# Optimization experiments

Measured on AMD Instinct MI355X. Metric: run time of the kernel, lower is better.

## Reference

```python
import jax, jax.numpy as jnp
import numpy as np

MEX_C = 2.0 / (np.sqrt(3.0) * np.pi ** 0.25)

def mexican_hat(z):
    return MEX_C * (z * z - 1.0) * jnp.exp(-0.5 * z * z)

def setup_inputs() -> dict:
    key = jax.random.key(0)
    ks = jax.random.split(key, 5)
    B, T, D, O = 4, 2048, 128, 128
    x = jax.random.normal(ks[0], (B, T, D), dtype=jnp.float32)
    # init like torch: scale ~ U(0.5,1.5), translation ~ U(-0.5,0.5), kaiming-ish weights
    scale = jax.random.uniform(ks[1], (O, D), dtype=jnp.float32, minval=0.5, maxval=1.5)
    translation = jax.random.uniform(ks[2], (O, D), dtype=jnp.float32, minval=-0.5, maxval=0.5)
    bound = 1.0 / np.sqrt(D)
    wavelet_weights = jax.random.uniform(ks[3], (O, D), dtype=jnp.float32, minval=-bound, maxval=bound)
    base_w = jax.random.uniform(ks[4], (O, D), dtype=jnp.float32, minval=-bound, maxval=bound)
    ln_gamma = jnp.ones((D,), dtype=jnp.float32)
    ln_beta = jnp.zeros((D,), dtype=jnp.float32)
    return {"x": x, "scale": scale, "translation": translation,
            "wavelet_weights": wavelet_weights, "base_w": base_w,
            "ln_gamma": ln_gamma, "ln_beta": ln_beta}

def reference(x, scale, translation, wavelet_weights, base_w, ln_gamma, ln_beta):
    B, T, D = x.shape
    O = wavelet_weights.shape[0]
    # LayerNorm over last dim (eps = 1e-5, torch default)
    mu = jnp.mean(x, axis=-1, keepdims=True)
    var = jnp.mean((x - mu) ** 2, axis=-1, keepdims=True)
    x_norm = (x - mu) / jnp.sqrt(var + 1e-5) * ln_gamma + ln_beta
    x_flat = x_norm.reshape(B * T, D)                      # (N, D)
    s = jax.nn.softplus(scale) + 0.1                       # (O, D)
    # broadcast intermediate (N, O, D) — the memory-bound path
    z = (x_flat[:, None, :] - translation[None]) / s[None]
    w = jnp.clip(mexican_hat(z), -10.0, 10.0)              # (N, O, D)
    wavelet_out = jnp.einsum('nod,od->no', w, wavelet_weights)
    base_out = x.reshape(B * T, D) @ base_w.T              # base uses raw x
    out = wavelet_out + jax.nn.silu(base_out)
    return out.reshape(B, T, O)
```

## Files before the change

### kernel.cpp

```cpp
#include <hip/hip_runtime.h>


#define D_DIM 128
#define O_DIM 128
#define ROWS  16
#define BLOCK 1024

#define C1     0.72134752f
#define SQRT_C 0.84932180f
#define WWK    1.2023651f
#define LOG2E  1.44269504f

__global__ __launch_bounds__(256) void wavekan_prep(
    const float* __restrict__ scale,
    const float* __restrict__ trans,
    const float* __restrict__ ww,
    const float* __restrict__ bw,
    float4* __restrict__ wsW)
{
    int idx = blockIdx.x * blockDim.x + threadIdx.x;
    if (idx >= O_DIM * D_DIM) return;
    int o = idx >> 7;
    int d = idx & (D_DIM - 1);
    float sc = scale[idx];
    float sp = fmaxf(sc, 0.0f) + log1pf(__expf(-fabsf(sc)));
    float is2 = SQRT_C / (sp + 0.1f);
    float4 w;
    w.x = trans[idx] * is2;
    w.y = is2;
    w.z = ww[idx] * WWK;
    w.w = bw[idx];
    wsW[d * O_DIM + o] = w;
}

template<bool USE_WS>
__global__ __launch_bounds__(BLOCK, 8) void wavekan_main(
    const float* __restrict__ x,
    const float* __restrict__ scale,
    const float* __restrict__ trans,
    const float* __restrict__ ww,
    const float* __restrict__ bw,
    const float* __restrict__ gamma,
    const float* __restrict__ beta,
    const float4* __restrict__ wsW,
    float* __restrict__ out,
    int N)
{
    __shared__ float2 s_lr[ROWS * D_DIM];

    const int tid  = threadIdx.x;
    const int row0 = blockIdx.x * ROWS;

    {
        const int r  = tid >> 6;
        const int j  = tid & 63;
        const int d0 = j * 2;
        const int grow = row0 + r;

        float2 v2 = make_float2(0.f, 0.f);
        if (grow < N)
            v2 = *reinterpret_cast<const float2*>(x + (size_t)grow * D_DIM + d0);

        float sum = v2.x + v2.y;
        float ssq = v2.x * v2.x + v2.y * v2.y;
        #pragma unroll
        for (int m = 1; m < 64; m <<= 1) {
            sum += __shfl_xor(sum, m, 64);
            ssq += __shfl_xor(ssq, m, 64);
        }
        const float mean = sum * (1.0f / D_DIM);
        const float var  = ssq * (1.0f / D_DIM) - mean * mean;
        const float rstd = rsqrtf(var + 1e-5f);

        float2 g2 = *reinterpret_cast<const float2*>(gamma + d0);
        float2 b2 = *reinterpret_cast<const float2*>(beta + d0);

        s_lr[r * D_DIM + d0]     = make_float2((v2.x - mean) * rstd * g2.x + b2.x, v2.x);
        s_lr[r * D_DIM + d0 + 1] = make_float2((v2.y - mean) * rstd * g2.y + b2.y, v2.y);
    }
    __syncthreads();

    const int o = tid & (O_DIM - 1);
    const int g = tid >> 7;
    const float2* __restrict__ lr = s_lr + g * 2 * D_DIM;

    float accw0 = 0.f, accw1 = 0.f, accb0 = 0.f, accb1 = 0.f;

    if (USE_WS) {
        float4 w = wsW[o];
        #pragma unroll 4
        for (int d = 0; d < D_DIM; ++d) {
            float4 wn = wsW[(((d + 1) & (D_DIM - 1)) << 7) + o];
            float2 v0 = lr[d];
            float2 v1 = lr[D_DIM + d];

            float u0 = fmaf(v0.x, w.y, -w.x);
            float u1 = fmaf(v1.x, w.y, -w.x);
            float q0 = u0 * u0;
            float q1 = u1 * u1;
            float e0 = __builtin_amdgcn_exp2f(-q0);
            float e1 = __builtin_amdgcn_exp2f(-q1);
            accw0 = fmaf((q0 - C1) * e0, w.z, accw0);
            accw1 = fmaf((q1 - C1) * e1, w.z, accw1);
            accb0 = fmaf(v0.y, w.w, accb0);
            accb1 = fmaf(v1.y, w.w, accb1);
            w = wn;
        }
    } else {
        for (int d = 0; d < D_DIM; ++d) {
            int idx = o * D_DIM + d;
            float sc = scale[idx];
            float sp = fmaxf(sc, 0.0f) + log1pf(__expf(-fabsf(sc)));
            float is  = SQRT_C / (sp + 0.1f);
            float tws = trans[idx] * is;
            float wwk = ww[idx] * WWK;
            float bwv = bw[idx];
            float2 v0 = lr[d];
            float2 v1 = lr[D_DIM + d];
            float u0 = fmaf(v0.x, is, -tws);
            float u1 = fmaf(v1.x, is, -tws);
            float q0 = u0 * u0;
            float q1 = u1 * u1;
            accw0 = fmaf((q0 - C1) * __builtin_amdgcn_exp2f(-q0), wwk, accw0);
            accw1 = fmaf((q1 - C1) * __builtin_amdgcn_exp2f(-q1), wwk, accw1);
            accb0 = fmaf(v0.y, bwv, accb0);
            accb1 = fmaf(v1.y, bwv, accb1);
        }
    }

    {
        const int rr0 = row0 + g * 2;
        if (rr0 < N) {
            float sig0 = 1.0f / (1.0f + __builtin_amdgcn_exp2f(-LOG2E * accb0));
            out[(size_t)rr0 * O_DIM + o] = accw0 + accb0 * sig0;
        }
        if (rr0 + 1 < N) {
            float sig1 = 1.0f / (1.0f + __builtin_amdgcn_exp2f(-LOG2E * accb1));
            out[(size_t)(rr0 + 1) * O_DIM + o] = accw1 + accb1 * sig1;
        }
    }
}

extern "C" void kernel_launch(void* const* d_in, const int* in_sizes, int n_in,
                              void* d_out, int out_size, void* d_ws, size_t ws_size,
                              hipStream_t stream) {
    const float* x     = (const float*)d_in[0];
    const float* scale = (const float*)d_in[1];
    const float* trans = (const float*)d_in[2];
    const float* ww    = (const float*)d_in[3];
    const float* bw    = (const float*)d_in[4];
    const float* gamma = (const float*)d_in[5];
    const float* beta  = (const float*)d_in[6];
    float* out = (float*)d_out;

    const int N = in_sizes[0] / D_DIM;
    const int grid = (N + ROWS - 1) / ROWS;

    const size_t ws_needed = (size_t)O_DIM * D_DIM * sizeof(float4);
    if (ws_size >= ws_needed) {
        wavekan_prep<<<(O_DIM * D_DIM + 255) / 256, 256, 0, stream>>>(
            scale, trans, ww, bw, (float4*)d_ws);
        wavekan_main<true><<<grid, BLOCK, 0, stream>>>(
            x, scale, trans, ww, bw, gamma, beta, (const float4*)d_ws, out, N);
    } else {
        wavekan_main<false><<<grid, BLOCK, 0, stream>>>(
            x, scale, trans, ww, bw, gamma, beta, nullptr, out, N);
    }
}
```

Before: 104.0 us.

## Stage weight chunks in LDS and vectorize two-row math with packed float2

The main loop now cooperatively loads 16-column chunks of the precomputed weight table into shared memory, register-prefetching the next chunk while computing on the current one. Before, each thread streamed its weights straight from global memory. The normalized and raw x values are re-laid out as float4 per (d, row-pair) with a padded stride to avoid bank conflicts. The two-row arithmetic uses ext_vector float2 types so the compiler can emit packed FP32 instructions. In exchange there are two extra block barriers per chunk and more LDS traffic. Shared memory use grows to about 50 KB per block.

After: 98.27 us. 5.5% less time.

```diff
diff --git a/kernel.cpp b/kernel.cpp
--- a/kernel.cpp
+++ b/kernel.cpp
@@ -5,11 +5,16 @@
 #define O_DIM 128
 #define ROWS  16
 #define BLOCK 1024
+#define CHUNK 16
+#define NCHUNK (D_DIM / CHUNK)
+#define XSTRIDE 9
 
 #define C1     0.72134752f
 #define SQRT_C 0.84932180f
 #define WWK    1.2023651f
 #define LOG2E  1.44269504f
+
+typedef float v2f __attribute__((ext_vector_type(2)));
 
 __global__ __launch_bounds__(256) void wavekan_prep(
     const float* __restrict__ scale,
@@ -46,7 +51,8 @@
     float* __restrict__ out,
     int N)
 {
-    __shared__ float2 s_lr[ROWS * D_DIM];
+    __shared__ float4 s_x[D_DIM * XSTRIDE];
+    __shared__ float4 s_w[CHUNK * O_DIM];
 
     const int tid  = threadIdx.x;
     const int row0 = blockIdx.x * ROWS;
@@ -75,38 +81,52 @@
         float2 g2 = *reinterpret_cast<const float2*>(gamma + d0);
         float2 b2 = *reinterpret_cast<const float2*>(beta + d0);
 
-        s_lr[r * D_DIM + d0]     = make_float2((v2.x - mean) * rstd * g2.x + b2.x, v2.x);
-        s_lr[r * D_DIM + d0 + 1] = make_float2((v2.y - mean) * rstd * g2.y + b2.y, v2.y);
+        const int p  = r >> 1;
+        const int h  = r & 1;
+        float* c0 = reinterpret_cast<float*>(&s_x[d0 * XSTRIDE + p]);
+        float* c1 = reinterpret_cast<float*>(&s_x[(d0 + 1) * XSTRIDE + p]);
+        c0[h]     = (v2.x - mean) * rstd * g2.x + b2.x;
+        c0[2 + h] = v2.x;
+        c1[h]     = (v2.y - mean) * rstd * g2.y + b2.y;
+        c1[2 + h] = v2.y;
     }
-    __syncthreads();
 
     const int o = tid & (O_DIM - 1);
     const int g = tid >> 7;
-    const float2* __restrict__ lr = s_lr + g * 2 * D_DIM;
 
-    float accw0 = 0.f, accw1 = 0.f, accb0 = 0.f, accb1 = 0.f;
+    v2f accw = {0.f, 0.f};
+    v2f accb = {0.f, 0.f};
 
     if (USE_WS) {
-        float4 w = wsW[o];
-        #pragma unroll 4
-        for (int d = 0; d < D_DIM; ++d) {
-            float4 wn = wsW[(((d + 1) & (D_DIM - 1)) << 7) + o];
-            float2 v0 = lr[d];
-            float2 v1 = lr[D_DIM + d];
+        float4 r0 = wsW[tid];
+        float4 r1 = wsW[tid + BLOCK];
+        for (int c = 0; c < NCHUNK; ++c) {
+            __syncthreads();
+            s_w[tid]         = r0;
+            s_w[tid + BLOCK] = r1;
+            if (c + 1 < NCHUNK) {
+                r0 = wsW[(c + 1) * (CHUNK * O_DIM) + tid];
+                r1 = wsW[(c + 1) * (CHUNK * O_DIM) + tid + BLOCK];
+            }
+            __syncthreads();
 
-            float u0 = fmaf(v0.x, w.y, -w.x);
-            float u1 = fmaf(v1.x, w.y, -w.x);
-            float q0 = u0 * u0;
-            float q1 = u1 * u1;
-            float e0 = __builtin_amdgcn_exp2f(-q0);
-            float e1 = __builtin_amdgcn_exp2f(-q1);
-            accw0 = fmaf((q0 - C1) * e0, w.z, accw0);
-            accw1 = fmaf((q1 - C1) * e1, w.z, accw1);
-            accb0 = fmaf(v0.y, w.w, accb0);
-            accb1 = fmaf(v1.y, w.w, accb1);
-            w = wn;
+            #pragma unroll
+            for (int dl = 0; dl < CHUNK; ++dl) {
+                float4 w  = s_w[dl * O_DIM + o];
+                float4 xx = s_x[(c * CHUNK + dl) * XSTRIDE + g];
+                v2f xln = {xx.x, xx.y};
+                v2f xrw = {xx.z, xx.w};
+                v2f u   = xln * w.y - w.x;
+                v2f q   = u * u;
+                v2f s1  = q - C1;
+                v2f e   = {__builtin_amdgcn_exp2f(-q.x),
+                           __builtin_amdgcn_exp2f(-q.y)};
+                accw += (s1 * e) * w.z;
+                accb += xrw * w.w;
+            }
         }
     } else {
+        __syncthreads();
         for (int d = 0; d < D_DIM; ++d) {
             int idx = o * D_DIM + d;
             float sc = scale[idx];
@@ -115,28 +135,28 @@
             float tws = trans[idx] * is;
             float wwk = ww[idx] * WWK;
             float bwv = bw[idx];
-            float2 v0 = lr[d];
-            float2 v1 = lr[D_DIM + d];
-            float u0 = fmaf(v0.x, is, -tws);
-            float u1 = fmaf(v1.x, is, -tws);
-            float q0 = u0 * u0;
-            float q1 = u1 * u1;
-            accw0 = fmaf((q0 - C1) * __builtin_amdgcn_exp2f(-q0), wwk, accw0);
-            accw1 = fmaf((q1 - C1) * __builtin_amdgcn_exp2f(-q1), wwk, accw1);
-            accb0 = fmaf(v0.y, bwv, accb0);
-            accb1 = fmaf(v1.y, bwv, accb1);
+            float4 xx = s_x[d * XSTRIDE + g];
+            v2f xln = {xx.x, xx.y};
+            v2f xrw = {xx.z, xx.w};
+            v2f u   = xln * is - tws;
+            v2f q   = u * u;
+            v2f s1  = q - C1;
+            v2f e   = {__builtin_amdgcn_exp2f(-q.x),
+                       __builtin_amdgcn_exp2f(-q.y)};
+            accw += (s1 * e) * wwk;
+            accb += xrw * bwv;
         }
     }
 
     {
         const int rr0 = row0 + g * 2;
         if (rr0 < N) {
-            float sig0 = 1.0f / (1.0f + __builtin_amdgcn_exp2f(-LOG2E * accb0));
-            out[(size_t)rr0 * O_DIM + o] = accw0 + accb0 * sig0;
+            float sig0 = 1.0f / (1.0f + __builtin_amdgcn_exp2f(-LOG2E * accb.x));
+            out[(size_t)rr0 * O_DIM + o] = accw.x + accb.x * sig0;
         }
         if (rr0 + 1 < N) {
-            float sig1 = 1.0f / (1.0f + __builtin_amdgcn_exp2f(-LOG2E * accb1));
-            out[(size_t)(rr0 + 1) * O_DIM + o] = accw1 + accb1 * sig1;
+            float sig1 = 1.0f / (1.0f + __builtin_amdgcn_exp2f(-LOG2E * accb.y));
+            out[(size_t)(rr0 + 1) * O_DIM + o] = accw.y + accb.y * sig1;
         }
     }
 }
```
